# Performance work log

Hardware: AMD Instinct MI355X
Metric: run time of the kernel (lower is better)

Reference implementation:

```python
import jax, jax.numpy as jnp
import numpy as np

D = 256

def setup_inputs() -> dict:
    key0 = jax.random.key(0)
    ks = jax.random.split(key0, 6)
    query = jax.random.normal(ks[0], (512, D), dtype=jnp.float32)
    key = jax.random.normal(ks[1], (1024, D), dtype=jnp.float32)
    value = jax.random.normal(ks[2], (1024, D), dtype=jnp.float32)
    # Linear weights (torch stores [out, in]; y = x @ W.T)
    W_q = jax.random.normal(ks[3], (D, D), dtype=jnp.float32) / np.sqrt(D)
    W_k = jax.random.normal(ks[4], (D, D), dtype=jnp.float32) / np.sqrt(D)
    v_w = jax.random.normal(ks[5], (1, D), dtype=jnp.float32) / np.sqrt(D)
    return {"query": query, "key": key, "value": value, "W_q": W_q, "W_k": W_k, "v_w": v_w}

def reference(query, key, value, W_q, W_k, v_w):
    # q_t: [Tq, D], k_t: [Tk, D]
    q_t = query @ W_q.T
    k_t = key @ W_k.T
    # combined: [Tq, Tk, D] broadcast; scores: [Tq, Tk] = tanh(q+k) @ v
    combined = jnp.tanh(q_t[:, None, :] + k_t[None, :, :])
    scores = jnp.einsum('qkd,d->qk', combined, v_w[0])
    return scores
```

## Files before the change

kernel.cpp:

```cpp
#include <hip/hip_runtime.h>

#define DD 256
#define TQ 512
#define TK 1024
#define NG 64
#define C2 2.88539008177792681472f

typedef short bf16x8 __attribute__((ext_vector_type(8)));
typedef short bf16x4 __attribute__((ext_vector_type(4)));
typedef float f32x4  __attribute__((ext_vector_type(4)));
typedef float f32x16 __attribute__((ext_vector_type(16)));

__device__ __forceinline__ float fexp2(float x){ return __builtin_amdgcn_exp2f(x); }
__device__ __forceinline__ float frcp (float x){ return __builtin_amdgcn_rcpf(x); }
__device__ __forceinline__ short rne_bf16(float x){
    union { float f; unsigned u; } v; v.f = x;
    unsigned r = v.u + 0x7FFFu + ((v.u >> 16) & 1u);
    return (short)(r >> 16);
}

__global__ __launch_bounds__(256) void proj_feat_kernel(
    const float* __restrict__ query, const float* __restrict__ key,
    const float* __restrict__ Wq, const float* __restrict__ Wk,
    const float* __restrict__ vw,
    unsigned short* __restrict__ phid, unsigned short* __restrict__ phin,
    unsigned short* __restrict__ psi)
{
    __shared__ short Wl[16 * 264];
    __shared__ short Xl[32 * 264];
    __shared__ float xch[2][64][5];
    __shared__ float et[2][16][21];

    const int tid = threadIdx.x;
    const int w = tid >> 6, l = tid & 63;
    const int ct = blockIdx.x & 15, chunk = blockIdx.x >> 4;
    const int qside = (chunk < 16);
    const float* X; const float* W; unsigned short* outd; int NT, tok0;
    if (qside) { X = query + chunk * 32 * DD; W = Wq; outd = phid; NT = TQ; tok0 = chunk * 32; }
    else { X = key + (chunk - 16) * 32 * DD; W = Wk; outd = psi; NT = TK; tok0 = (chunk - 16) * 32; }
    const float* Wp0 = W + ct * 16 * DD;

    #pragma unroll
    for (int rep = 0; rep < 4; ++rep) {
        int idx = rep * 256 + tid;
        float4 f4 = ((const float4*)Wp0)[idx];
        int row = idx >> 6, dc = (idx & 63) * 4;
        bf16x4 b = { rne_bf16(f4.x), rne_bf16(f4.y), rne_bf16(f4.z), rne_bf16(f4.w) };
        *(bf16x4*)&Wl[row * 264 + dc] = b;
    }
    #pragma unroll
    for (int rep = 0; rep < 8; ++rep) {
        int idx = rep * 256 + tid;
        float4 f4 = ((const float4*)X)[idx];
        int row = idx >> 6, dc = (idx & 63) * 4;
        bf16x4 b = { rne_bf16(f4.x), rne_bf16(f4.y), rne_bf16(f4.z), rne_bf16(f4.w) };
        *(bf16x4*)&Xl[row * 264 + dc] = b;
    }
    __syncthreads();

    const int pair = w >> 1, khalf = w & 1;
    const int lr = l & 15, kg = (l >> 4) * 8;
    const int arow = pair * 16 + lr;

    f32x4 acc = {0.f, 0.f, 0.f, 0.f};
    #pragma unroll
    for (int k0 = 0; k0 < 4; ++k0) {
        const int kk = khalf * 128 + k0 * 32 + kg;
        bf16x8 af = *(const bf16x8*)&Xl[arow * 264 + kk];
        bf16x8 bf = *(const bf16x8*)&Wl[lr * 264 + kk];
        acc = __builtin_amdgcn_mfma_f32_16x16x32_bf16(af, bf, acc, 0, 0, 0);
    }

    if (khalf == 1) {
        #pragma unroll
        for (int r = 0; r < 4; ++r) xch[pair][l][r] = acc[r];
    }
    __syncthreads();
    if (khalf == 0) {
        #pragma unroll
        for (int r = 0; r < 4; ++r) acc[r] += xch[pair][l][r];

        float* etp = &et[pair][0][0];
        #pragma unroll
        for (int r = 0; r < 4; ++r)
            etp[lr * 21 + (l >> 4) * 4 + r] = fexp2(C2 * acc[r]);

        const int tl = l & 15, gq = l >> 4;
        float E0 = etp[(gq * 4 + 0) * 21 + tl];
        float E1 = etp[(gq * 4 + 1) * 21 + tl];
        float E2 = etp[(gq * 4 + 2) * 21 + tl];
        float E3 = etp[(gq * 4 + 3) * 21 + tl];
        float p[16];
        p[0]=1.f;   p[1]=E0;      p[2]=E1;      p[3]=E0*E1;
        p[4]=E2;    p[5]=E0*E2;   p[6]=E1*E2;   p[7]=p[3]*E2;
        p[8]=E3;    p[9]=E0*E3;   p[10]=E1*E3;  p[11]=p[3]*E3;
        p[12]=E2*E3;p[13]=p[5]*E3;p[14]=p[6]*E3;p[15]=p[7]*E3;

        const int g = ct * 4 + gq;
        const int token = tok0 + pair * 16 + tl;
        const int base = (g * NT + token) * 16;
        bf16x8 w0, w1;
        #pragma unroll
        for (int j = 0; j < 8; ++j) { w0[j] = rne_bf16(p[j]); w1[j] = rne_bf16(p[8+j]); }
        *(bf16x8*)&outd[base]     = w0;
        *(bf16x8*)&outd[base + 8] = w1;

        if (qside) {
            float4 v4 = *(const float4*)&vw[4 * g];
            float v0 = v4.x, v1 = v4.y, v2 = v4.z, v3 = v4.w;
            float sall = v0 + v1 + v2 + v3;
            float c[16];
            c[0]=sall;      c[1]=sall-v0;      c[2]=sall-v1;      c[3]=c[1]-v1;
            c[4]=sall-v2;   c[5]=c[1]-v2;      c[6]=c[2]-v2;      c[7]=c[3]-v2;
            c[8]=sall-v3;   c[9]=c[1]-v3;      c[10]=c[2]-v3;     c[11]=c[3]-v3;
            c[12]=c[4]-v3;  c[13]=c[5]-v3;     c[14]=c[6]-v3;     c[15]=0.f;
            bf16x8 n0, n1;
            #pragma unroll
            for (int j = 0; j < 8; ++j) { n0[j] = rne_bf16(c[j]*p[j]); n1[j] = rne_bf16(c[8+j]*p[8+j]); }
            *(bf16x8*)&phin[base]     = n0;
            *(bf16x8*)&phin[base + 8] = n1;
        }
    }
}

#define MERGE16(NA, DA, NQ, DQ) { f32x16 _t = (NQ) * (DA); (NA) = (NA) * (DQ) + _t; (DA) = (DA) * (DQ); }

__global__ __launch_bounds__(512, 2) void scores_kernel(
    const unsigned short* __restrict__ phid, const unsigned short* __restrict__ phin,
    const unsigned short* __restrict__ psi,  const float* __restrict__ vw,
    float* __restrict__ out)
{
    __shared__ float red[8][64][17];
    __shared__ float vsum_s;
    const int id = blockIdx.x;
    const int qb = (id & 7) + 8 * (id >> 8);
    const int kb = (id >> 3) & 31;
    const int tid = threadIdx.x;
    const int w = tid >> 6, l = tid & 63, lr31 = l & 31, lh = l >> 5;

    if (tid < 64) {
        float4 vv = *(const float4*)&vw[tid * 4];
        float s = vv.x + vv.y + vv.z + vv.w;
        #pragma unroll
        for (int m = 1; m < 64; m <<= 1) s += __shfl_xor(s, m);
        if (tid == 0) vsum_s = s;
    }

    const int qt = qb * 32 + lr31;
    const int kt = kb * 32 + lr31;
    const int fo = lh * 8;
    const f32x16 z = {0.f,0.f,0.f,0.f,0.f,0.f,0.f,0.f,0.f,0.f,0.f,0.f,0.f,0.f,0.f,0.f};

    f32x16 a = z;
    #pragma unroll
    for (int hx = 0; hx < 2; ++hx) {
        f32x16 nA, dA;
        #pragma unroll
        for (int qi = 0; qi < 4; ++qi) {
            const int g = w * 8 + hx * 4 + qi;
            bf16x8 afd = *(const bf16x8*)&phid[(g * TQ + qt) * 16 + fo];
            bf16x8 afn = *(const bf16x8*)&phin[(g * TQ + qt) * 16 + fo];
            bf16x8 bp  = *(const bf16x8*)&psi [(g * TK + kt) * 16 + fo];
            f32x16 d = __builtin_amdgcn_mfma_f32_32x32x16_bf16(afd, bp, z, 0, 0, 0);
            f32x16 n = __builtin_amdgcn_mfma_f32_32x32x16_bf16(afn, bp, z, 0, 0, 0);
            if (qi == 0) { nA = n; dA = d; }
            else MERGE16(nA, dA, n, d);
        }
        #pragma unroll
        for (int r = 0; r < 16; ++r)
            a[r] = fmaf(nA[r], frcp(dA[r]), a[r]);
    }

    #pragma unroll
    for (int r = 0; r < 16; ++r) red[w][l][r] = a[r];
    __syncthreads();

    const float vsum = vsum_s;
    const int lane = tid & 63, rbase = (tid >> 6) * 2;
    const int lane_lh = lane >> 5, lane_lr = lane & 31;
    #pragma unroll
    for (int rr = 0; rr < 2; ++rr) {
        const int r = rbase + rr;
        float sum = 0.f;
        #pragma unroll
        for (int ww = 0; ww < 8; ++ww) sum += red[ww][lane][r];
        const int row = qb * 32 + (r & 3) + 8 * (r >> 2) + 4 * lane_lh;
        const int col = kb * 32 + lane_lr;
        out[row * TK + col] = fmaf(-2.f, sum, vsum);
    }
}

extern "C" void kernel_launch(void* const* d_in, const int* in_sizes, int n_in,
                              void* d_out, int out_size, void* d_ws, size_t ws_size,
                              hipStream_t stream) {
    const float* query = (const float*)d_in[0];
    const float* key   = (const float*)d_in[1];
    const float* Wq    = (const float*)d_in[3];
    const float* Wk    = (const float*)d_in[4];
    const float* vw    = (const float*)d_in[5];
    float* out = (float*)d_out;

    char* ws = (char*)d_ws;
    unsigned short* phid = (unsigned short*)ws;
    unsigned short* phin = (unsigned short*)(ws + 1048576);
    unsigned short* psi  = (unsigned short*)(ws + 2097152);

    proj_feat_kernel<<<768, 256, 0, stream>>>(query, key, Wq, Wk, vw, phid, phin, psi);
    scores_kernel<<<512, 512, 0, stream>>>(phid, phin, psi, vw, out);
}
```

Baseline: 19.09 us.

## Use 1024-thread blocks with 16 waves per group and 64-key tiles in scores kernel

Restructures the scores kernel so each block covers a 32x64 output tile with 16 waves, each wave owning 4 feature groups instead of 8. The query-side fragments are loaded once into registers and reused across two 32-key subtiles. Cross-wave reduction becomes a two-stage shared-memory add, which needs several extra barriers. The grid drops to 256 blocks of 1024 threads, raising per-wave parallelism over groups and requesting higher occupancy, at the cost of more register pressure and more synchronisation.

Result: slower. 30.58 us (+60.2%).

```diff
diff --git a/kernel.cpp b/kernel.cpp
--- a/kernel.cpp
+++ b/kernel.cpp
@@ -125,16 +125,14 @@
 
 #define MERGE16(NA, DA, NQ, DQ) { f32x16 _t = (NQ) * (DA); (NA) = (NA) * (DQ) + _t; (DA) = (DA) * (DQ); }
 
-__global__ __launch_bounds__(512, 2) void scores_kernel(
+__global__ __launch_bounds__(1024, 4) void scores_kernel(
     const unsigned short* __restrict__ phid, const unsigned short* __restrict__ phin,
     const unsigned short* __restrict__ psi,  const float* __restrict__ vw,
     float* __restrict__ out)
 {
     __shared__ float red[8][64][17];
     __shared__ float vsum_s;
-    const int id = blockIdx.x;
-    const int qb = (id & 7) + 8 * (id >> 8);
-    const int kb = (id >> 3) & 31;
+    const int qb = blockIdx.x & 15, kb = blockIdx.x >> 4;
     const int tid = threadIdx.x;
     const int w = tid >> 6, l = tid & 63, lr31 = l & 31, lh = l >> 5;
 
@@ -146,46 +144,85 @@
         if (tid == 0) vsum_s = s;
     }
 
-    const int qt = qb * 32 + lr31;
-    const int kt = kb * 32 + lr31;
-    const int fo = lh * 8;
+    const int qt  = qb * 32 + lr31;
+    const int kt0 = kb * 64 + lr31;
+    const int fo  = lh * 8;
     const f32x16 z = {0.f,0.f,0.f,0.f,0.f,0.f,0.f,0.f,0.f,0.f,0.f,0.f,0.f,0.f,0.f,0.f};
-
-    f32x16 a = z;
-    #pragma unroll
-    for (int hx = 0; hx < 2; ++hx) {
+    const int g0 = w * 4;
+
+    bf16x8 afd[4], afn[4];
+    #pragma unroll
+    for (int qi = 0; qi < 4; ++qi) {
+        afd[qi] = *(const bf16x8*)&phid[((g0 + qi) * TQ + qt) * 16 + fo];
+        afn[qi] = *(const bf16x8*)&phin[((g0 + qi) * TQ + qt) * 16 + fo];
+    }
+
+    f32x16 a0, a1;
+    {
         f32x16 nA, dA;
         #pragma unroll
         for (int qi = 0; qi < 4; ++qi) {
-            const int g = w * 8 + hx * 4 + qi;
-            bf16x8 afd = *(const bf16x8*)&phid[(g * TQ + qt) * 16 + fo];
-            bf16x8 afn = *(const bf16x8*)&phin[(g * TQ + qt) * 16 + fo];
-            bf16x8 bp  = *(const bf16x8*)&psi [(g * TK + kt) * 16 + fo];
-            f32x16 d = __builtin_amdgcn_mfma_f32_32x32x16_bf16(afd, bp, z, 0, 0, 0);
-            f32x16 n = __builtin_amdgcn_mfma_f32_32x32x16_bf16(afn, bp, z, 0, 0, 0);
+            bf16x8 bp = *(const bf16x8*)&psi[((g0 + qi) * TK + kt0) * 16 + fo];
+            f32x16 d = __builtin_amdgcn_mfma_f32_32x32x16_bf16(afd[qi], bp, z, 0, 0, 0);
+            f32x16 n = __builtin_amdgcn_mfma_f32_32x32x16_bf16(afn[qi], bp, z, 0, 0, 0);
             if (qi == 0) { nA = n; dA = d; }
             else MERGE16(nA, dA, n, d);
         }
         #pragma unroll
-        for (int r = 0; r < 16; ++r)
-            a[r] = fmaf(nA[r], frcp(dA[r]), a[r]);
-    }
-
-    #pragma unroll
-    for (int r = 0; r < 16; ++r) red[w][l][r] = a[r];
-    __syncthreads();
+        for (int r = 0; r < 16; ++r) a0[r] = nA[r] * frcp(dA[r]);
+    }
+    {
+        f32x16 nA, dA;
+        #pragma unroll
+        for (int qi = 0; qi < 4; ++qi) {
+            bf16x8 bp = *(const bf16x8*)&psi[((g0 + qi) * TK + kt0 + 32) * 16 + fo];
+            f32x16 d = __builtin_amdgcn_mfma_f32_32x32x16_bf16(afd[qi], bp, z, 0, 0, 0);
+            f32x16 n = __builtin_amdgcn_mfma_f32_32x32x16_bf16(afn[qi], bp, z, 0, 0, 0);
+            if (qi == 0) { nA = n; dA = d; }
+            else MERGE16(nA, dA, n, d);
+        }
+        #pragma unroll
+        for (int r = 0; r < 16; ++r) a1[r] = nA[r] * frcp(dA[r]);
+    }
 
     const float vsum = vsum_s;
-    const int lane = tid & 63, rbase = (tid >> 6) * 2;
-    const int lane_lh = lane >> 5, lane_lr = lane & 31;
-    #pragma unroll
-    for (int rr = 0; rr < 2; ++rr) {
-        const int r = rbase + rr;
+    if (w >= 8) {
+        #pragma unroll
+        for (int r = 0; r < 16; ++r) red[w - 8][l][r] = a0[r];
+    }
+    __syncthreads();
+    if (w < 8) {
+        #pragma unroll
+        for (int r = 0; r < 16; ++r) red[w][l][r] += a0[r];
+    }
+    __syncthreads();
+    {
+        const int r = w;
         float sum = 0.f;
         #pragma unroll
-        for (int ww = 0; ww < 8; ++ww) sum += red[ww][lane][r];
-        const int row = qb * 32 + (r & 3) + 8 * (r >> 2) + 4 * lane_lh;
-        const int col = kb * 32 + lane_lr;
+        for (int ww = 0; ww < 8; ++ww) sum += red[ww][l][r];
+        const int row = qb * 32 + (r & 3) + 8 * (r >> 2) + 4 * lh;
+        const int col = kb * 64 + lr31;
+        out[row * TK + col] = fmaf(-2.f, sum, vsum);
+    }
+    __syncthreads();
+    if (w >= 8) {
+        #pragma unroll
+        for (int r = 0; r < 16; ++r) red[w - 8][l][r] = a1[r];
+    }
+    __syncthreads();
+    if (w < 8) {
+        #pragma unroll
+        for (int r = 0; r < 16; ++r) red[w][l][r] += a1[r];
+    }
+    __syncthreads();
+    {
+        const int r = w;
+        float sum = 0.f;
+        #pragma unroll
+        for (int ww = 0; ww < 8; ++ww) sum += red[ww][l][r];
+        const int row = qb * 32 + (r & 3) + 8 * (r >> 2) + 4 * lh;
+        const int col = kb * 64 + 32 + lr31;
         out[row * TK + col] = fmaf(-2.f, sum, vsum);
     }
 }
@@ -206,5 +243,5 @@
     unsigned short* psi  = (unsigned short*)(ws + 2097152);
 
     proj_feat_kernel<<<768, 256, 0, stream>>>(query, key, Wq, Wk, vw, phid, phin, psi);
-    scores_kernel<<<512, 512, 0, stream>>>(phid, phin, psi, vw, out);
-}
+    scores_kernel<<<256, 1024, 0, stream>>>(phid, phin, psi, vw, out);
+}
```
